# Kernel optimization log

Hardware: AMD Instinct MI355X
Metric: run time of the kernel (lower is better)

The kernel has to match this reference:

```python
import jax, jax.numpy as jnp
import numpy as np

N_NODES = 100000
N_EDGES = 1600000
HIDDEN = 64
N_MID = 3  # num_layers=5 -> 1 first + 3 middle + 1 last


def setup_inputs() -> dict:
    key = jax.random.key(0)
    ks = jax.random.split(key, 12)
    x = jax.random.normal(ks[0], (N_NODES, 1), dtype=jnp.float32)
    edge_index = jax.random.randint(ks[1], (2, N_EDGES), 0, N_NODES, dtype=jnp.int32)
    edge_weight = jax.random.uniform(ks[2], (N_EDGES,), dtype=jnp.float32)
    s0 = 1.0  # fan_in=1
    sh = 1.0 / np.sqrt(HIDDEN)
    Wrel0 = jax.random.normal(ks[3], (HIDDEN, 1), dtype=jnp.float32) * s0
    brel0 = jax.random.normal(ks[4], (HIDDEN,), dtype=jnp.float32) * s0
    Wroot0 = jax.random.normal(ks[5], (HIDDEN, 1), dtype=jnp.float32) * s0
    Wrel_mid = jax.random.normal(ks[6], (N_MID, HIDDEN, HIDDEN), dtype=jnp.float32) * sh
    brel_mid = jax.random.normal(ks[7], (N_MID, HIDDEN), dtype=jnp.float32) * sh
    Wroot_mid = jax.random.normal(ks[8], (N_MID, HIDDEN, HIDDEN), dtype=jnp.float32) * sh
    WrelL = jax.random.normal(ks[9], (1, HIDDEN), dtype=jnp.float32) * sh
    brelL = jax.random.normal(ks[10], (1,), dtype=jnp.float32) * sh
    WrootL = jax.random.normal(ks[11], (1, HIDDEN), dtype=jnp.float32) * sh
    return {"x": x, "edge_index": edge_index, "edge_weight": edge_weight,
            "Wrel0": Wrel0, "brel0": brel0, "Wroot0": Wroot0,
            "Wrel_mid": Wrel_mid, "brel_mid": brel_mid, "Wroot_mid": Wroot_mid,
            "WrelL": WrelL, "brelL": brelL, "WrootL": WrootL}


def reference(x, edge_index, edge_weight, Wrel0, brel0, Wroot0,
              Wrel_mid, brel_mid, Wroot_mid, WrelL, brelL, WrootL):
    src = edge_index[0]
    dst = edge_index[1]
    n = x.shape[0]

    def conv(h, Wrel, brel, Wroot):
        # PyG GraphConv(aggr='add'): lin_rel(sum_j w_ij * h_j) + lin_root(h_i)
        msg = h[src] * edge_weight[:, None]          # [E, C]
        agg = jax.ops.segment_sum(msg, dst, num_segments=n)  # [N, C]
        return agg @ Wrel.T + brel + h @ Wroot.T

    # dropout omitted (deterministic reference); relu after all but last layer
    h = jax.nn.relu(conv(x, Wrel0, brel0, Wroot0))
    for i in range(Wrel_mid.shape[0]):
        h = jax.nn.relu(conv(h, Wrel_mid[i], brel_mid[i], Wroot_mid[i]))
    return conv(h, WrelL, brelL, WrootL)  # [N, 1]
```

## Files before the change

kernel.cpp:

```cpp
#include <hip/hip_runtime.h>
#include <stdint.h>


#define NN 100000
#define NE 1600000
#define HID 64
#define NBKT 391
#define CAP 8192
#define TILE 4096
#define EPT 16
#define NTILE ((NE + TILE - 1) / TILE)

typedef __attribute__((ext_vector_type(8))) short bf16x8;
typedef __attribute__((ext_vector_type(4))) float f32x4;

__device__ __forceinline__ uint32_t rne_bf16(float v) {
    uint32_t u = __float_as_uint(v);
    return (u + 0x7fffu + ((u >> 16) & 1u)) >> 16;
}


__global__ __launch_bounds__(256) void k_bpart(const int* __restrict__ src,
                                               const int* __restrict__ dst,
                                               const float* __restrict__ w,
                                               int* __restrict__ bcur,
                                               int2* __restrict__ bpairs) {
    __shared__ int  hcnt[NBKT];
    __shared__ int  hoff[NBKT];
    __shared__ int  hadj[NBKT];
    __shared__ int  sc0[512];
    __shared__ int  sc1[512];
    __shared__ int2 sT[TILE];
    __shared__ int  sAdj[TILE];
    int tile0 = blockIdx.x * TILE;
    int t = threadIdx.x;
    for (int i = t; i < NBKT; i += 256) hcnt[i] = 0;
    __syncthreads();

    int   pk[EPT];
    int   bk[EPT];
    float wv[EPT];
    #pragma unroll
    for (int k = 0; k < EPT; k++) {
        int e = tile0 + t + k * 256;
        if (e < NE) {
            int d = dst[e];
            int b = d >> 8;
            pk[k] = (src[e] << 8) | (d & 255);
            wv[k] = w[e];
            bk[k] = b;
            atomicAdd(&hcnt[b], 1);
        } else {
            bk[k] = -1;
        }
    }
    __syncthreads();

    sc0[t]       = (t < NBKT) ? hcnt[t] : 0;
    sc0[t + 256] = (t + 256 < NBKT) ? hcnt[t + 256] : 0;
    __syncthreads();
    int* cur = sc0;
    int* oth = sc1;
    for (int off = 1; off < 512; off <<= 1) {
        int v0 = cur[t]       + ((t       >= off) ? cur[t - off]       : 0);
        int v1 = cur[t + 256] + ((t + 256 >= off) ? cur[t + 256 - off] : 0);
        oth[t] = v0;
        oth[t + 256] = v1;
        __syncthreads();
        int* tmp = cur; cur = oth; oth = tmp;
    }
    for (int i = t; i < NBKT; i += 256) {
        int c = hcnt[i];
        int excl = cur[i] - c;
        hoff[i] = excl;
        int gbase = c ? atomicAdd(&bcur[i], c) : 0;
        hadj[i] = gbase - excl;
        hcnt[i] = 0;
    }
    __syncthreads();

    #pragma unroll
    for (int k = 0; k < EPT; k++) {
        if (bk[k] >= 0) {
            int b = bk[k];
            int pos = hoff[b] + atomicAdd(&hcnt[b], 1);
            sT[pos] = make_int2(pk[k], __float_as_int(wv[k]));
            sAdj[pos] = hadj[b];
        }
    }
    __syncthreads();

    int n = NE - tile0; if (n > TILE) n = TILE;
    for (int j = t; j < n; j += 256)
        bpairs[sAdj[j] + j] = sT[j];
}

__global__ __launch_bounds__(256) void k_bcsr(const int* __restrict__ bcur,
                                              const int2* __restrict__ bpairs,
                                              int* __restrict__ offs,
                                              int* __restrict__ ends,
                                              uint32_t* __restrict__ pairs) {
    __shared__ int2 sE[CAP];
    __shared__ int cnt[256];
    __shared__ int scn[256];
    __shared__ int cur[256];
    int k = blockIdx.x, t = threadIdx.x;
    int base = k * CAP;
    int scnt = bcur[k] - base;
    cnt[t] = 0;
    __syncthreads();
    for (int j = t; j < scnt; j += 256) {
        int2 q = bpairs[base + j];
        sE[j] = q;
        atomicAdd(&cnt[q.x & 255], 1);
    }
    __syncthreads();
    int v = cnt[t], acc = v;
    scn[t] = v;
    __syncthreads();
    for (int off = 1; off < 256; off <<= 1) {
        int u = (t >= off) ? scn[t - off] : 0;
        __syncthreads();
        acc += u;
        scn[t] = acc;
        __syncthreads();
    }
    int excl = acc - v;
    cur[t] = excl;
    int d = (k << 8) + t;
    if (d < NN) {
        offs[d] = base + excl;
        ends[d] = base + excl + v;
    }
    __syncthreads();
    for (int j = t; j < scnt; j += 256) {
        int2 q = sE[j];
        int pos = base + atomicAdd(&cur[q.x & 255], 1);
        uint32_t wb = rne_bf16(__int_as_float(q.y)) & 0x7fffu;
        pairs[pos] = (wb << 17) | (uint32_t)(q.x >> 8);
    }
}


__global__ __launch_bounds__(256) void k_wsplit(const float* __restrict__ Wrel_mid,
                                                const float* __restrict__ Wroot_mid,
                                                uint16_t* __restrict__ WgH,
                                                uint16_t* __restrict__ WgL,
                                                uint16_t* __restrict__ WrH,
                                                uint16_t* __restrict__ WrL,
                                                int* __restrict__ bcur) {
    int i = blockIdx.x * blockDim.x + threadIdx.x;
    if (i < NBKT) bcur[i] = i * CAP;
    if (i >= 3 * 4096) return;
    float a = Wrel_mid[i];
    uint32_t ah = rne_bf16(a);
    float al = a - __uint_as_float(ah << 16);
    WgH[i] = (uint16_t)ah;
    WgL[i] = (uint16_t)rne_bf16(al);
    float b = Wroot_mid[i];
    uint32_t bh = rne_bf16(b);
    float bl = b - __uint_as_float(bh << 16);
    WrH[i] = (uint16_t)bh;
    WrL[i] = (uint16_t)rne_bf16(bl);
}


__device__ __forceinline__ void mfma_epilogue(
        int lane, int w, const uint32_t* sH,
        const uint16_t* __restrict__ WgH, const uint16_t* __restrict__ WgL,
        const uint16_t* __restrict__ WrH, const uint16_t* __restrict__ WrL,
        const float* __restrict__ brel,
        uint16_t* sG, uint16_t* sR) {
    int row = lane & 15;
    int quad = lane >> 4;
    int kb = quad * 8;
    bf16x8 ah0 = *(const bf16x8*)&sH[row * 36 + quad * 4];
    bf16x8 ah1 = *(const bf16x8*)&sH[row * 36 + 16 + quad * 4];
    int oc = w * 16 + row;
    {
        bf16x8 bh0 = *(const bf16x8*)&WgH[oc * 64 + kb];
        bf16x8 bh1 = *(const bf16x8*)&WgH[oc * 64 + 32 + kb];
        bf16x8 bl0 = *(const bf16x8*)&WgL[oc * 64 + kb];
        bf16x8 bl1 = *(const bf16x8*)&WgL[oc * 64 + 32 + kb];
        f32x4 acc = {0.f, 0.f, 0.f, 0.f};
        acc = __builtin_amdgcn_mfma_f32_16x16x32_bf16(ah0, bh0, acc, 0, 0, 0);
        acc = __builtin_amdgcn_mfma_f32_16x16x32_bf16(ah1, bh1, acc, 0, 0, 0);
        acc = __builtin_amdgcn_mfma_f32_16x16x32_bf16(ah0, bl0, acc, 0, 0, 0);
        acc = __builtin_amdgcn_mfma_f32_16x16x32_bf16(ah1, bl1, acc, 0, 0, 0);
        #pragma unroll
        for (int r = 0; r < 4; r++)
            sG[(quad * 4 + r) * 68 + oc] = (uint16_t)rne_bf16(acc[r]);
    }
    {
        bf16x8 bh0 = *(const bf16x8*)&WrH[oc * 64 + kb];
        bf16x8 bh1 = *(const bf16x8*)&WrH[oc * 64 + 32 + kb];
        bf16x8 bl0 = *(const bf16x8*)&WrL[oc * 64 + kb];
        bf16x8 bl1 = *(const bf16x8*)&WrL[oc * 64 + 32 + kb];
        float bias = brel[oc];
        f32x4 acc = {bias, bias, bias, bias};
        acc = __builtin_amdgcn_mfma_f32_16x16x32_bf16(ah0, bh0, acc, 0, 0, 0);
        acc = __builtin_amdgcn_mfma_f32_16x16x32_bf16(ah1, bh1, acc, 0, 0, 0);
        acc = __builtin_amdgcn_mfma_f32_16x16x32_bf16(ah0, bl0, acc, 0, 0, 0);
        acc = __builtin_amdgcn_mfma_f32_16x16x32_bf16(ah1, bl1, acc, 0, 0, 0);
        #pragma unroll
        for (int r = 0; r < 4; r++)
            sR[(quad * 4 + r) * 68 + oc] = (uint16_t)rne_bf16(acc[r]);
    }
}

__device__ __forceinline__ void epilogue_writeout(
        int tid, int blk16, const uint16_t* sG, const uint16_t* sR,
        uint16_t* __restrict__ Gout, uint16_t* __restrict__ Rout) {
    const uint32_t* sGd = (const uint32_t*)sG;
    const uint32_t* sRd = (const uint32_t*)sR;
    uint32_t* Gd = (uint32_t*)Gout;
    uint32_t* Rd = (uint32_t*)Rout;
    #pragma unroll
    for (int it = 0; it < 2; it++) {
        int idx = it * 256 + tid;
        int nd = idx >> 5, col = idx & 31;
        Gd[(blk16 + nd) * 32 + col] = sGd[nd * 34 + col];
        Rd[(blk16 + nd) * 32 + col] = sRd[nd * 34 + col];
    }
}


__global__ __launch_bounds__(256) void k_l0pre(
        const int* __restrict__ offs, const int* __restrict__ ends,
        const uint32_t* __restrict__ pairs, const float* __restrict__ x,
        const float* __restrict__ Wrel0, const float* __restrict__ brel0,
        const float* __restrict__ Wroot0,
        const uint16_t* __restrict__ WgH, const uint16_t* __restrict__ WgL,
        const uint16_t* __restrict__ WrH, const uint16_t* __restrict__ WrL,
        const float* __restrict__ brel,
        uint16_t* __restrict__ Gout, uint16_t* __restrict__ Rout) {
    __shared__ uint32_t sH[16 * 36];
    __shared__ uint16_t sG[16 * 68];
    __shared__ uint16_t sR[16 * 68];
    int c = threadIdx.x & 63;
    int w = threadIdx.x >> 6;
    int blk16 = blockIdx.x * 16;
    float agg[4];
    #pragma unroll
    for (int t = 0; t < 4; t++) {
        int node = blk16 + w * 4 + t;
        int b = offs[node], e = ends[node];
        float pp = 0.f;
        for (int j = b + c; j < e; j += 64) {
            uint32_t r = pairs[j];
            pp += __uint_as_float((r >> 17) << 16) * x[r & 0x1ffffu];
        }
        for (int o = 32; o > 0; o >>= 1) pp += __shfl_down(pp, o, 64);
        agg[t] = __shfl(pp, 0, 64);
    }
    float wr = Wrel0[c], br = brel0[c], wo = Wroot0[c];
    #pragma unroll
    for (int t = 0; t < 4; t++) {
        int node = blk16 + w * 4 + t;
        float v = agg[t] * wr + br + x[node] * wo;
        v = v > 0.f ? v : 0.f;
        uint32_t hb = rne_bf16(v);
        uint32_t pn = (uint32_t)__shfl_xor((int)hb, 1, 64);
        if (!(c & 1)) sH[(w * 4 + t) * 36 + (c >> 1)] = hb | (pn << 16);
    }
    __syncthreads();
    mfma_epilogue(c, w, sH, WgH, WgL, WrH, WrL, brel, sG, sR);
    __syncthreads();
    epilogue_writeout((int)threadIdx.x, blk16, sG, sR, Gout, Rout);
}

template <bool LAST>
__global__ __launch_bounds__(256, 4) void k_aggfused(
        const int* __restrict__ offs, const int* __restrict__ ends,
        const uint32_t* __restrict__ pairs,
        const uint16_t* __restrict__ Gb, const uint16_t* __restrict__ Rb,
        const uint16_t* __restrict__ WgH, const uint16_t* __restrict__ WgL,
        const uint16_t* __restrict__ WrH, const uint16_t* __restrict__ WrL,
        const float* __restrict__ brel,
        uint16_t* __restrict__ Gout, uint16_t* __restrict__ Rout,
        const float* __restrict__ WrelL, const float* __restrict__ WrootL,
        float* __restrict__ sarr, float* __restrict__ rarr) {
    __shared__ uint32_t sH[16 * 36];
    __shared__ uint16_t sG[16 * 68];
    __shared__ uint16_t sR[16 * 68];
    int c = threadIdx.x & 63;
    int w = threadIdx.x >> 6;
    int blk16 = blockIdx.x * 16;
    int n0 = blk16 + w * 4;
    int ov = 0;
    if (c < 4) ov = offs[n0 + c];
    else if (c == 4) ov = ends[n0 + 3];
    int bnd[5];
    bnd[0] = __builtin_amdgcn_readlane(ov, 0);
    bnd[1] = __builtin_amdgcn_readlane(ov, 1);
    bnd[2] = __builtin_amdgcn_readlane(ov, 2);
    bnd[3] = __builtin_amdgcn_readlane(ov, 3);
    bnd[4] = __builtin_amdgcn_readlane(ov, 4);

    uint32_t ur[4];
    #pragma unroll
    for (int t = 0; t < 4; t++) ur[t] = Rb[(n0 + t) * 64 + c];

    float acc[4][4];
    #pragma unroll
    for (int t = 0; t < 4; t++)
        #pragma unroll
        for (int q = 0; q < 4; q++) acc[t][q] = 0.f;

    for (int cb = bnd[0]; cb < bnd[4]; cb += 64) {
        int n = bnd[4] - cb; if (n > 64) n = 64;
        uint32_t p = (c < n) ? pairs[cb + c] : 0u;
        #pragma unroll
        for (int t = 0; t < 4; t++) {
            int lo = bnd[t]     > cb     ? bnd[t]     : cb;
            int hi = bnd[t + 1] < cb + n ? bnd[t + 1] : cb + n;
            int j = lo;
            for (; j + 16 <= hi; j += 16) {
                int jj = j - cb;
                uint32_t rr[16], uu[16];
                #pragma unroll
                for (int q = 0; q < 16; q++)
                    rr[q] = __builtin_amdgcn_readlane(p, jj + q);
                #pragma unroll
                for (int q = 0; q < 16; q++)
                    uu[q] = Gb[(rr[q] & 0x1ffffu) * 64 + c];
                #pragma unroll
                for (int q = 0; q < 16; q++)
                    acc[t][q & 3] += __uint_as_float((rr[q] >> 17) << 16)
                                   * __uint_as_float(uu[q] << 16);
            }
            for (; j + 8 <= hi; j += 8) {
                int jj = j - cb;
                uint32_t rr[8], uu[8];
                #pragma unroll
                for (int q = 0; q < 8; q++)
                    rr[q] = __builtin_amdgcn_readlane(p, jj + q);
                #pragma unroll
                for (int q = 0; q < 8; q++)
                    uu[q] = Gb[(rr[q] & 0x1ffffu) * 64 + c];
                #pragma unroll
                for (int q = 0; q < 8; q++)
                    acc[t][q & 3] += __uint_as_float((rr[q] >> 17) << 16)
                                   * __uint_as_float(uu[q] << 16);
            }
            for (; j + 4 <= hi; j += 4) {
                int jj = j - cb;
                uint32_t rr[4], uu[4];
                #pragma unroll
                for (int q = 0; q < 4; q++)
                    rr[q] = __builtin_amdgcn_readlane(p, jj + q);
                #pragma unroll
                for (int q = 0; q < 4; q++)
                    uu[q] = Gb[(rr[q] & 0x1ffffu) * 64 + c];
                #pragma unroll
                for (int q = 0; q < 4; q++)
                    acc[t][q] += __uint_as_float((rr[q] >> 17) << 16)
                               * __uint_as_float(uu[q] << 16);
            }
            for (; j < hi; j++) {
                int jj = j - cb;
                uint32_t r = __builtin_amdgcn_readlane(p, jj);
                uint32_t u = Gb[(r & 0x1ffffu) * 64 + c];
                acc[t][0] += __uint_as_float((r >> 17) << 16)
                           * __uint_as_float(u << 16);
            }
        }
    }
    #pragma unroll
    for (int t = 0; t < 4; t++) {
        float v = (acc[t][0] + acc[t][1]) + (acc[t][2] + acc[t][3])
                + __uint_as_float(ur[t] << 16);
        v = v > 0.f ? v : 0.f;
        if (!LAST) {
            uint32_t hb = rne_bf16(v);
            uint32_t pn = (uint32_t)__shfl_xor((int)hb, 1, 64);
            if (!(c & 1)) sH[(w * 4 + t) * 36 + (c >> 1)] = hb | (pn << 16);
        } else {
            float a = v * WrelL[c];
            float r = v * WrootL[c];
            for (int o = 32; o > 0; o >>= 1) {
                a += __shfl_down(a, o, 64);
                r += __shfl_down(r, o, 64);
            }
            if (c == 0) { sarr[n0 + t] = a; rarr[n0 + t] = r; }
        }
    }
    if (!LAST) {
        __syncthreads();
        mfma_epilogue(c, w, sH, WgH, WgL, WrH, WrL, brel, sG, sR);
        __syncthreads();
        epilogue_writeout((int)threadIdx.x, blk16, sG, sR, Gout, Rout);
    }
}

__global__ void k_last(const int* __restrict__ offs, const int* __restrict__ ends,
                       const uint32_t* __restrict__ pairs,
                       const float* __restrict__ sarr, const float* __restrict__ rarr,
                       const float* __restrict__ brelL, float* __restrict__ out) {
    int i = blockIdx.x * blockDim.x + threadIdx.x;
    if (i >= NN) return;
    float a0 = rarr[i] + brelL[0], a1 = 0.f;
    int b = offs[i], e = ends[i];
    int j = b;
    for (; j + 2 <= e; j += 2) {
        uint32_t r0 = pairs[j], r1 = pairs[j + 1];
        a0 += __uint_as_float((r0 >> 17) << 16) * sarr[r0 & 0x1ffffu];
        a1 += __uint_as_float((r1 >> 17) << 16) * sarr[r1 & 0x1ffffu];
    }
    for (; j < e; j++) {
        uint32_t r = pairs[j];
        a0 += __uint_as_float((r >> 17) << 16) * sarr[r & 0x1ffffu];
    }
    out[i] = a0 + a1;
}

extern "C" void kernel_launch(void* const* d_in, const int* in_sizes, int n_in,
                              void* d_out, int out_size, void* d_ws, size_t ws_size,
                              hipStream_t stream) {
    const float* x        = (const float*)d_in[0];
    const int*   ei       = (const int*)d_in[1];
    const float* ew       = (const float*)d_in[2];
    const float* Wrel0    = (const float*)d_in[3];
    const float* brel0    = (const float*)d_in[4];
    const float* Wroot0   = (const float*)d_in[5];
    const float* Wrel_mid = (const float*)d_in[6];
    const float* brel_mid = (const float*)d_in[7];
    const float* Wroot_mid= (const float*)d_in[8];
    const float* WrelL    = (const float*)d_in[9];
    const float* brelL    = (const float*)d_in[10];
    const float* WrootL   = (const float*)d_in[11];
    float* out = (float*)d_out;

    const int* src  = ei;
    const int* dstp = ei + NE;

    char* w = (char*)d_ws;
    size_t o = 0;
    auto alloc = [&](size_t b) -> void* {
        void* r = (void*)(w + o);
        o += (b + 255) & ~(size_t)255;
        return r;
    };
    int*      offs  = (int*)alloc((size_t)NN * 4);
    int*      ends  = (int*)alloc((size_t)NN * 4);
    int*      bcur  = (int*)alloc((size_t)NBKT * 4);
    uint16_t* WgH   = (uint16_t*)alloc((size_t)3 * 4096 * 2);
    uint16_t* WgL   = (uint16_t*)alloc((size_t)3 * 4096 * 2);
    uint16_t* WrH   = (uint16_t*)alloc((size_t)3 * 4096 * 2);
    uint16_t* WrL   = (uint16_t*)alloc((size_t)3 * 4096 * 2);
    float*    sarr  = (float*)alloc((size_t)NN * 4);
    float*    rarr  = (float*)alloc((size_t)NN * 4);
    uint32_t* pairs = (uint32_t*)alloc((size_t)NBKT * CAP * 4);
    uint16_t* GbA   = (uint16_t*)alloc((size_t)NN * HID * 2);
    uint16_t* RbA   = (uint16_t*)alloc((size_t)NN * HID * 2);
    uint16_t* GbB   = (uint16_t*)alloc((size_t)NN * HID * 2);
    uint16_t* RbB   = (uint16_t*)alloc((size_t)NN * HID * 2);
    (void)RbB;
    int2*  bpairs = (int2*)GbB;

    k_wsplit<<<(3 * 4096 + 255) / 256, 256, 0, stream>>>(
        Wrel_mid, Wroot_mid, WgH, WgL, WrH, WrL, bcur);

    k_bpart<<<NTILE, 256, 0, stream>>>(src, dstp, ew, bcur, bpairs);
    k_bcsr<<<NBKT, 256, 0, stream>>>(bcur, bpairs, offs, ends, pairs);

    k_l0pre<<<NN / 16, 256, 0, stream>>>(
        offs, ends, pairs, x, Wrel0, brel0, Wroot0,
        WgH, WgL, WrH, WrL, brel_mid, GbA, RbA);

    k_aggfused<false><<<NN / 16, 256, 0, stream>>>(
        offs, ends, pairs, GbA, RbA,
        WgH + 4096, WgL + 4096, WrH + 4096, WrL + 4096, brel_mid + HID,
        GbB, RbB, WrelL, WrootL, sarr, rarr);
    k_aggfused<false><<<NN / 16, 256, 0, stream>>>(
        offs, ends, pairs, GbB, RbB,
        WgH + 2 * 4096, WgL + 2 * 4096, WrH + 2 * 4096, WrL + 2 * 4096,
        brel_mid + 2 * HID, GbA, RbA, WrelL, WrootL, sarr, rarr);
    k_aggfused<true><<<NN / 16, 256, 0, stream>>>(
        offs, ends, pairs, GbA, RbA,
        WgH, WgL, WrH, WrL, brel_mid,
        GbB, RbB, WrelL, WrootL, sarr, rarr);

    k_last<<<(NN + 255) / 256, 256, 0, stream>>>(offs, ends, pairs, sarr, rarr, brelL, out);
}
```

Measured before the change: 326.8 us.

## Stage neighbor feature rows into LDS via direct global-to-LDS loads

Replaces per-lane 2-byte scattered gathers of neighbor feature rows with 16-byte global_load_lds transfers that copy whole 128-byte rows into a per-wave LDS staging buffer in 32-edge chunks, then reads the features from LDS for the weighted accumulation. It also prefetches the next 64 packed edge pairs while the current batch is processed. The aim is fewer, wider memory transactions in the gather. In exchange it adds about 16KB of LDS per block, which may lower occupancy, and a full vmcnt(0) wait per chunk that serializes load and compute within each wave.

```diff
diff --git a/kernel.cpp b/kernel.cpp
--- a/kernel.cpp
+++ b/kernel.cpp
@@ -10,6 +10,7 @@
 #define TILE 4096
 #define EPT 16
 #define NTILE ((NE + TILE - 1) / TILE)
+#define CHUNK 32
 
 typedef __attribute__((ext_vector_type(8))) short bf16x8;
 typedef __attribute__((ext_vector_type(4))) float f32x4;
@@ -283,6 +284,7 @@
     __shared__ uint32_t sH[16 * 36];
     __shared__ uint16_t sG[16 * 68];
     __shared__ uint16_t sR[16 * 68];
+    __shared__ __align__(128) uint16_t sStage[4][CHUNK * 64];
     int c = threadIdx.x & 63;
     int w = threadIdx.x >> 6;
     int blk16 = blockIdx.x * 16;
@@ -307,65 +309,79 @@
         #pragma unroll
         for (int q = 0; q < 4; q++) acc[t][q] = 0.f;
 
+    uint16_t* stg = sStage[w];
+    const char* gbase = (const char*)Gb;
+    int lg4   = (c >> 3) * 4;
+    int lbyte = (c & 7) * 16;
+
+    uint32_t p = 0;
+    if (bnd[0] + c < bnd[4]) p = pairs[bnd[0] + c];
+
     for (int cb = bnd[0]; cb < bnd[4]; cb += 64) {
-        int n = bnd[4] - cb; if (n > 64) n = 64;
-        uint32_t p = (c < n) ? pairs[cb + c] : 0u;
+        uint32_t pn = 0;
+        if (cb + 64 + c < bnd[4]) pn = pairs[cb + 64 + c];
         #pragma unroll
-        for (int t = 0; t < 4; t++) {
-            int lo = bnd[t]     > cb     ? bnd[t]     : cb;
-            int hi = bnd[t + 1] < cb + n ? bnd[t + 1] : cb + n;
-            int j = lo;
-            for (; j + 16 <= hi; j += 16) {
-                int jj = j - cb;
-                uint32_t rr[16], uu[16];
+        for (int s = 0; s < 2; s++) {
+            int sb = cb + s * 32;
+            if (sb < bnd[4]) {
+                int sn = bnd[4] - sb; if (sn > 32) sn = 32;
+                int ni = (sn + 7) >> 3;
                 #pragma unroll
-                for (int q = 0; q < 16; q++)
-                    rr[q] = __builtin_amdgcn_readlane(p, jj + q);
+                for (int i = 0; i < 4; i++) {
+                    if (i < ni) {
+                        int idx = (s * 32 + i * 8) * 4 + lg4;
+                        uint32_t r = (uint32_t)__builtin_amdgcn_ds_bpermute(idx, (int)p);
+                        uint32_t voff = ((r & 0x1ffffu) << 7) + (uint32_t)lbyte;
+                        __builtin_amdgcn_global_load_lds(
+                            (const __attribute__((address_space(1))) void*)(gbase + voff),
+                            (__attribute__((address_space(3))) void*)((char*)stg + i * 1024),
+                            16, 0, 0);
+                    }
+                }
+                asm volatile("s_waitcnt vmcnt(0)" ::: "memory");
                 #pragma unroll
-                for (int q = 0; q < 16; q++)
-                    uu[q] = Gb[(rr[q] & 0x1ffffu) * 64 + c];
-                #pragma unroll
-                for (int q = 0; q < 16; q++)
-                    acc[t][q & 3] += __uint_as_float((rr[q] >> 17) << 16)
-                                   * __uint_as_float(uu[q] << 16);
-            }
-            for (; j + 8 <= hi; j += 8) {
-                int jj = j - cb;
-                uint32_t rr[8], uu[8];
-                #pragma unroll
-                for (int q = 0; q < 8; q++)
-                    rr[q] = __builtin_amdgcn_readlane(p, jj + q);
-                #pragma unroll
-                for (int q = 0; q < 8; q++)
-                    uu[q] = Gb[(rr[q] & 0x1ffffu) * 64 + c];
-                #pragma unroll
-                for (int q = 0; q < 8; q++)
-                    acc[t][q & 3] += __uint_as_float((rr[q] >> 17) << 16)
-                                   * __uint_as_float(uu[q] << 16);
-            }
-            for (; j + 4 <= hi; j += 4) {
-                int jj = j - cb;
-                uint32_t rr[4], uu[4];
-                #pragma unroll
-                for (int q = 0; q < 4; q++)
-                    rr[q] = __builtin_amdgcn_readlane(p, jj + q);
-                #pragma unroll
-                for (int q = 0; q < 4; q++)
-                    uu[q] = Gb[(rr[q] & 0x1ffffu) * 64 + c];
-                #pragma unroll
-                for (int q = 0; q < 4; q++)
-                    acc[t][q] += __uint_as_float((rr[q] >> 17) << 16)
-                               * __uint_as_float(uu[q] << 16);
-            }
-            for (; j < hi; j++) {
-                int jj = j - cb;
-                uint32_t r = __builtin_amdgcn_readlane(p, jj);
-                uint32_t u = Gb[(r & 0x1ffffu) * 64 + c];
-                acc[t][0] += __uint_as_float((r >> 17) << 16)
-                           * __uint_as_float(u << 16);
+                for (int t = 0; t < 4; t++) {
+                    int lo = bnd[t] > sb ? bnd[t] : sb;
+                    int hi = bnd[t + 1] < sb + sn ? bnd[t + 1] : sb + sn;
+                    int j = lo;
+                    for (; j + 8 <= hi; j += 8) {
+                        uint32_t rr[8], gg[8];
+                        #pragma unroll
+                        for (int q = 0; q < 8; q++)
+                            rr[q] = __builtin_amdgcn_readlane(p, j - cb + q);
+                        #pragma unroll
+                        for (int q = 0; q < 8; q++)
+                            gg[q] = (uint32_t)stg[(j - sb + q) * 64 + c];
+                        #pragma unroll
+                        for (int q = 0; q < 8; q++)
+                            acc[t][q & 3] += __uint_as_float((rr[q] >> 17) << 16)
+                                           * __uint_as_float(gg[q] << 16);
+                    }
+                    for (; j + 4 <= hi; j += 4) {
+                        uint32_t rr[4], gg[4];
+                        #pragma unroll
+                        for (int q = 0; q < 4; q++)
+                            rr[q] = __builtin_amdgcn_readlane(p, j - cb + q);
+                        #pragma unroll
+                        for (int q = 0; q < 4; q++)
+                            gg[q] = (uint32_t)stg[(j - sb + q) * 64 + c];
+                        #pragma unroll
+                        for (int q = 0; q < 4; q++)
+                            acc[t][q] += __uint_as_float((rr[q] >> 17) << 16)
+                                       * __uint_as_float(gg[q] << 16);
+                    }
+                    for (; j < hi; j++) {
+                        uint32_t r = __builtin_amdgcn_readlane(p, j - cb);
+                        uint32_t g = (uint32_t)stg[(j - sb) * 64 + c];
+                        acc[t][0] += __uint_as_float((r >> 17) << 16)
+                                   * __uint_as_float(g << 16);
+                    }
+                }
             }
         }
-    }
+        p = pn;
+    }
+
     #pragma unroll
     for (int t = 0; t < 4; t++) {
         float v = (acc[t][0] + acc[t][1]) + (acc[t][2] + acc[t][3])
@@ -373,8 +389,8 @@
         v = v > 0.f ? v : 0.f;
         if (!LAST) {
             uint32_t hb = rne_bf16(v);
-            uint32_t pn = (uint32_t)__shfl_xor((int)hb, 1, 64);
-            if (!(c & 1)) sH[(w * 4 + t) * 36 + (c >> 1)] = hb | (pn << 16);
+            uint32_t pn2 = (uint32_t)__shfl_xor((int)hb, 1, 64);
+            if (!(c & 1)) sH[(w * 4 + t) * 36 + (c >> 1)] = hb | (pn2 << 16);
         } else {
             float a = v * WrelL[c];
             float r = v * WrootL[c];
```

Measured after the change: 311.0 us. 4.8% less time.
